# Optimization experiments

Measured on AMD Instinct MI355X. Metric: run time of the kernel, lower is better.

Reference implementation:

```python
import jax, jax.numpy as jnp
import numpy as np

B, IN, H0, H1, OUT = 4096, 1024, 4096, 4096, 1024
QMAX = 127.0


def setup_inputs() -> dict:
    key = jax.random.key(0)
    k0, k1, k2, k3 = jax.random.split(key, 4)
    x = jax.random.normal(k0, (B, IN), dtype=jnp.float32)
    # Linear weights hold already-quantized integer values (module casts .int())
    W0 = jax.random.randint(k1, (H0, IN + 1), -127, 128).astype(jnp.int32)
    W1 = jax.random.randint(k2, (H1, H0 + 1), -127, 128).astype(jnp.int32)
    W2 = jax.random.randint(k3, (OUT, H1 + 1), -127, 128).astype(jnp.int32)
    return {
        "x": x,
        "a_in0": jnp.float32(4.0), "a_w0": jnp.float32(0.05),
        "a_in2": jnp.float32(50.0), "a_w2": jnp.float32(0.05),
        "a_in4": jnp.float32(50.0), "a_w4": jnp.float32(0.05),
        "W0": W0, "W1": W1, "W2": W2,
    }


def _quant(x, amax):
    # clamp(round(x * 127/amax), -127, 127) -> int32
    return jnp.clip(jnp.round(x * (QMAX / amax)), -QMAX, QMAX).astype(jnp.int32)


def _qlinear(x, W, a_in, a_w):
    q = _quant(x, a_in)                                   # [B, K] int32
    ones = jnp.ones((q.shape[0], 1), dtype=jnp.int32)     # folded bias column
    q = jnp.concatenate([q, ones], axis=1)                # [B, K+1]
    acc = q @ W.T                                         # int32 GEMM [B, N]
    return acc.astype(jnp.float32) * (a_w * a_in / (QMAX * QMAX))


def reference(x, a_in0, a_w0, a_in2, a_w2, a_in4, a_w4, W0, W1, W2):
    x = x.reshape(x.shape[0], -1)
    x = _qlinear(x, W0, a_in0, a_w0)
    x = jax.nn.relu(x)
    x = _qlinear(x, W1, a_in2, a_w2)
    x = jax.nn.relu(x)
    x = _qlinear(x, W2, a_in4, a_w4)
    return x
```

## Files before the change

### kernel.cpp

```cpp
#include <hip/hip_runtime.h>

#define QMAX 127.0f

typedef int v4i __attribute__((ext_vector_type(4)));

__device__ __forceinline__ void gload_lds16(const void* g, void* l) {
  __builtin_amdgcn_global_load_lds(
      (const __attribute__((address_space(1))) void*)g,
      (__attribute__((address_space(3))) void*)l, 16, 0, 0);
}

__device__ __forceinline__ void pack_body(const int* __restrict__ W,
                                          signed char* __restrict__ W8,
                                          int* __restrict__ bias,
                                          unsigned lblk, int kshift) {
  unsigned t = lblk * 256u + threadIdx.x;
  unsigned row = t >> kshift;
  unsigned j = t & ((1u << kshift) - 1u);
  unsigned K = 4u << kshift;
  size_t srcBase = (size_t)row * (size_t)(K + 1) + (size_t)j * 4;
  int c0 = W[srcBase + 0], c1 = W[srcBase + 1], c2 = W[srcBase + 2], c3 = W[srcBase + 3];
  unsigned packed = (unsigned)(c0 & 0xff) | ((unsigned)(c1 & 0xff) << 8) |
                    ((unsigned)(c2 & 0xff) << 16) | ((unsigned)(c3 & 0xff) << 24);
  reinterpret_cast<unsigned*>(W8)[t] = packed;
  if (j == 0) bias[row] = W[(size_t)row * (K + 1) + K];
}

__global__ void prep_kernel(const float* __restrict__ x,
                            signed char* __restrict__ qa0,
                            const float* __restrict__ pAin,
                            const int* __restrict__ W0, signed char* __restrict__ W0p, int* __restrict__ b0,
                            const int* __restrict__ W1, signed char* __restrict__ W1p, int* __restrict__ b1,
                            const int* __restrict__ W2, signed char* __restrict__ W2p, int* __restrict__ b2) {
  unsigned blk = blockIdx.x;
  if (blk < 4096u) {
    pack_body(W0, W0p, b0, blk, 8);
  } else if (blk < 20480u) {
    pack_body(W1, W1p, b1, blk - 4096u, 10);
  } else if (blk < 24576u) {
    pack_body(W2, W2p, b2, blk - 20480u, 10);
  } else {
    unsigned t = (blk - 24576u) * 256u + threadIdx.x;
    float s = QMAX / pAin[0];
    float4 v = reinterpret_cast<const float4*>(x)[t];
    int q0 = (int)fminf(fmaxf(rintf(v.x * s), -QMAX), QMAX);
    int q1 = (int)fminf(fmaxf(rintf(v.y * s), -QMAX), QMAX);
    int q2 = (int)fminf(fmaxf(rintf(v.z * s), -QMAX), QMAX);
    int q3 = (int)fminf(fmaxf(rintf(v.w * s), -QMAX), QMAX);
    unsigned packed = (unsigned)(q0 & 0xff) | ((unsigned)(q1 & 0xff) << 8) |
                      ((unsigned)(q2 & 0xff) << 16) | ((unsigned)(q3 & 0xff) << 24);
    reinterpret_cast<unsigned*>(qa0)[t] = packed;
  }
}


#define FENCE() asm volatile("" ::: "memory")
#define BARRIER()                      \
  do {                                 \
    FENCE();                           \
    __builtin_amdgcn_s_barrier();      \
    FENCE();                           \
  } while (0)
#define LGK0() asm volatile("s_waitcnt lgkmcnt(0)" ::: "memory")
#define VMC8() asm volatile("s_waitcnt vmcnt(8)" ::: "memory")
#define VMC0() asm volatile("s_waitcnt vmcnt(0)" ::: "memory")

#define STAGE_A(bf, h, t)                                                     \
  do {                                                                        \
    const signed char* _g = gA + (size_t)((h) * 128) * K + (size_t)(t) * 128; \
    signed char* _l = ldsA + (bf) * 32768 + (h) * 16384 + ldsThr;             \
    gload_lds16(_g, _l);                                                      \
    gload_lds16(_g + (size_t)8 * K, _l + 1024);                               \
  } while (0)

#define STAGE_B(bf, h, t)                                                     \
  do {                                                                        \
    const signed char* _g = gB + (size_t)((h) * 128) * K + (size_t)(t) * 128; \
    signed char* _l = ldsB + (bf) * 32768 + (h) * 16384 + ldsThr;             \
    gload_lds16(_g, _l);                                                      \
    gload_lds16(_g + (size_t)8 * K, _l + 1024);                               \
  } while (0)

#define LDAQ(bf, qm)                                                          \
  do {                                                                        \
    _Pragma("unroll") for (int m = 0; m < 4; ++m) {                           \
      int row = wm * 128 + (qm) * 64 + m * 16 + l15;                          \
      _Pragma("unroll") for (int kk = 0; kk < 2; ++kk) {                      \
        int off = (kk * 64 + hi * 16) ^ ((row & 7) << 4);                     \
        aq[m][kk] = *(const v4i*)(ldsA + (bf) * 32768 + row * 128 + off);     \
      }                                                                       \
    }                                                                         \
  } while (0)

#define LDBF(bf)                                                              \
  do {                                                                        \
    _Pragma("unroll") for (int n = 0; n < 4; ++n) {                           \
      int row = wn * 64 + n * 16 + l15;                                       \
      _Pragma("unroll") for (int kk = 0; kk < 2; ++kk) {                      \
        int off = (kk * 64 + hi * 16) ^ ((row & 7) << 4);                     \
        bR[n][kk] = *(const v4i*)(ldsB + (bf) * 32768 + row * 128 + off);     \
      }                                                                       \
    }                                                                         \
  } while (0)

#define MFMAC(qm)                                                             \
  do {                                                                        \
    __builtin_amdgcn_s_setprio(1);                                            \
    _Pragma("unroll") for (int m = 0; m < 4; ++m)                             \
    _Pragma("unroll") for (int n = 0; n < 4; ++n)                             \
    _Pragma("unroll") for (int kk = 0; kk < 2; ++kk)                          \
      acc[(qm) * 4 + m][n] = __builtin_amdgcn_mfma_i32_16x16x64_i8(           \
          aq[m][kk], bR[n][kk], acc[(qm) * 4 + m][n], 0, 0, 0);               \
    __builtin_amdgcn_s_setprio(0);                                            \
  } while (0)

__global__ __launch_bounds__(512, 2)
void qgemm256_kernel(const signed char* __restrict__ A,
                     const signed char* __restrict__ Bw,
                     const int* __restrict__ bias,
                     signed char* __restrict__ O,
                     int N, int K, int nbn,
                     const float* __restrict__ pAin,
                     const float* __restrict__ pAw,
                     const float* __restrict__ pAnext) {
  extern __shared__ signed char lds[];
  signed char* ldsA = lds;
  signed char* ldsB = lds + 65536;

  const int nwg = gridDim.x, bid = blockIdx.x, per = nwg >> 3;
  const int swz = (bid & 7) * per + (bid >> 3);
  const int brow = swz / nbn, bcol = swz - brow * nbn;
  const int browBase = brow << 8, bcolBase = bcol << 8;

  const int tid = threadIdx.x;
  const int lane = tid & 63, l15 = lane & 15, hi = lane >> 4;
  const int wid = tid >> 6, wm = wid >> 2, wn = wid & 3;

  const int rloc = (wid << 4) + (lane >> 3);
  const int csrc = (lane & 7) ^ ((lane >> 3) & 7);
  const signed char* gA = A + (size_t)(browBase + rloc) * K + csrc * 16;
  const signed char* gB = Bw + (size_t)(bcolBase + rloc) * K + csrc * 16;
  const int ldsThr = (wid << 11) + lane * 16;

  v4i acc[8][4] = {};
  v4i bR[4][2];

  const int nk = K >> 7, niter = nk >> 1, nkm = nk - 1;

  STAGE_B(0, 0, 0); STAGE_B(0, 1, 0); STAGE_A(0, 0, 0); STAGE_A(0, 1, 0);
  STAGE_B(1, 0, 1); STAGE_B(1, 1, 1);

#pragma unroll 1
  for (int i = 0; i < niter; ++i) {
    const int t1 = 2 * i + 1;
    const int tE = (2 * i + 2) & nkm;
    const int tO = (2 * i + 3) & nkm;
    v4i aq[4][2];
    STAGE_A(1, 0, t1); STAGE_A(1, 1, t1);
    VMC8();
    BARRIER();
    LDAQ(0, 0); LDBF(0);
    MFMAC(0);
    LGK0();
    BARRIER();
    STAGE_B(0, 0, tE); STAGE_B(0, 1, tE);
    LDAQ(0, 1);
    MFMAC(1);
    LGK0();
    BARRIER();
    STAGE_A(0, 0, tE); STAGE_A(0, 1, tE);
    VMC8();
    BARRIER();
    LDAQ(1, 0); LDBF(1);
    MFMAC(0);
    LGK0();
    BARRIER();
    STAGE_B(1, 0, tO); STAGE_B(1, 1, tO);
    LDAQ(1, 1);
    MFMAC(1);
    LGK0();
    BARRIER();
  }

  VMC0();

  const float sDeq = (pAw[0] * pAin[0]) / (QMAX * QMAX);
  const float sQ = QMAX / pAnext[0];
#pragma unroll
  for (int nf = 0; nf < 4; ++nf) {
    const int gcol = bcolBase + wn * 64 + nf * 16 + l15;
    const int bv = bias[gcol];
#pragma unroll
    for (int mf = 0; mf < 8; ++mf) {
      const int gr = browBase + wm * 128 + mf * 16 + (hi << 2);
#pragma unroll
      for (int r = 0; r < 4; ++r) {
        float f = (float)(acc[mf][nf][r] + bv) * sDeq;
        f = fmaxf(f, 0.0f);
        float qf = fminf(fmaxf(rintf(f * sQ), -QMAX), QMAX);
        O[(size_t)(gr + r) * N + gcol] = (signed char)(int)qf;
      }
    }
  }
}

__global__ __launch_bounds__(256)
void qgemm_kernel(const signed char* __restrict__ A,
                  const signed char* __restrict__ Bw,
                  const int* __restrict__ bias,
                  float* __restrict__ O,
                  int N, int K, int nbn,
                  const float* __restrict__ pAin,
                  const float* __restrict__ pAw) {
  __shared__ signed char slds[32768];
  signed char* ldsA = slds;
  signed char* ldsB = slds + 16384;

  int nwg = gridDim.x;
  int bid = blockIdx.x;
  int per = nwg >> 3;
  int swz = (bid & 7) * per + (bid >> 3);
  int brow = swz / nbn;
  int bcol = swz - brow * nbn;
  int browBase = brow << 7;
  int bcolBase = bcol << 7;

  int tid = threadIdx.x;
  int lane = tid & 63;
  int l15 = lane & 15;
  int hi = lane >> 4;
  int wid = tid >> 6;
  int wr = (wid >> 1) << 6;
  int wc = (wid & 1) << 6;

  v4i acc[4][4] = {};

  int nk = K >> 7;
  for (int kt = 0; kt < nk; ++kt) {
    int k0 = kt << 7;
#pragma unroll
    for (int i = 0; i < 4; ++i) {
      int c = i * 256 + tid;
      int r = c >> 3;
      int osrc = ((c & 7) << 4) ^ ((r & 7) << 4);
      gload_lds16(A + (size_t)(browBase + r) * K + (k0 + osrc), ldsA + c * 16);
      gload_lds16(Bw + (size_t)(bcolBase + r) * K + (k0 + osrc), ldsB + c * 16);
    }
    __syncthreads();
#pragma unroll
    for (int kk = 0; kk < 2; ++kk) {
      v4i a[4], b[4];
#pragma unroll
      for (int m = 0; m < 4; ++m) {
        int row = wr + m * 16 + l15;
        int off = (kk * 64 + hi * 16) ^ ((row & 7) << 4);
        a[m] = *reinterpret_cast<const v4i*>(ldsA + row * 128 + off);
      }
#pragma unroll
      for (int n = 0; n < 4; ++n) {
        int row = wc + n * 16 + l15;
        int off = (kk * 64 + hi * 16) ^ ((row & 7) << 4);
        b[n] = *reinterpret_cast<const v4i*>(ldsB + row * 128 + off);
      }
#pragma unroll
      for (int m = 0; m < 4; ++m)
#pragma unroll
        for (int n = 0; n < 4; ++n)
          acc[m][n] = __builtin_amdgcn_mfma_i32_16x16x64_i8(a[m], b[n], acc[m][n], 0, 0, 0);
    }
    __syncthreads();
  }

  float sDeq = (pAw[0] * pAin[0]) / (QMAX * QMAX);
#pragma unroll
  for (int n = 0; n < 4; ++n) {
    int gcol = bcolBase + wc + n * 16 + l15;
    int bv = bias[gcol];
#pragma unroll
    for (int m = 0; m < 4; ++m) {
      int growb = browBase + wr + m * 16 + (hi << 2);
#pragma unroll
      for (int r = 0; r < 4; ++r) {
        O[(size_t)(growb + r) * N + gcol] = (float)(acc[m][n][r] + bv) * sDeq;
      }
    }
  }
}

extern "C" void kernel_launch(void* const* d_in, const int* in_sizes, int n_in,
                              void* d_out, int out_size, void* d_ws, size_t ws_size,
                              hipStream_t stream) {
  const float* x     = (const float*)d_in[0];
  const float* a_in0 = (const float*)d_in[1];
  const float* a_w0  = (const float*)d_in[2];
  const float* a_in2 = (const float*)d_in[3];
  const float* a_w2  = (const float*)d_in[4];
  const float* a_in4 = (const float*)d_in[5];
  const float* a_w4  = (const float*)d_in[6];
  const int*   W0    = (const int*)d_in[7];
  const int*   W1    = (const int*)d_in[8];
  const int*   W2    = (const int*)d_in[9];
  float* out = (float*)d_out;

  constexpr int B = 4096, IN = 1024, H0 = 4096, H1 = 4096, OUTN = 1024;

  char* ws = (char*)d_ws;
  size_t off = 0;
  auto alloc = [&](size_t sz) {
    char* p = ws + off;
    off += (sz + 255) & ~(size_t)255;
    return p;
  };
  signed char* qa0 = (signed char*)alloc((size_t)B * IN);
  signed char* qa1 = (signed char*)alloc((size_t)B * H0);
  signed char* qa2 = (signed char*)alloc((size_t)B * H1);
  signed char* W0p = (signed char*)alloc((size_t)H0 * IN);
  signed char* W1p = (signed char*)alloc((size_t)H1 * H0);
  signed char* W2p = (signed char*)alloc((size_t)OUTN * H1);
  int* b0 = (int*)alloc((size_t)H0 * 4);
  int* b1 = (int*)alloc((size_t)H1 * 4);
  int* b2 = (int*)alloc((size_t)OUTN * 4);

  hipFuncSetAttribute((const void*)qgemm256_kernel,
                      hipFuncAttributeMaxDynamicSharedMemorySize, 131072);

  prep_kernel<<<28672, 256, 0, stream>>>(x, qa0, a_in0,
                                         W0, W0p, b0,
                                         W1, W1p, b1,
                                         W2, W2p, b2);

  qgemm256_kernel<<<(B / 256) * (H0 / 256), 512, 131072, stream>>>(
      qa0, W0p, b0, qa1, H0, IN, H0 / 256, a_in0, a_w0, a_in2);

  qgemm256_kernel<<<(B / 256) * (H1 / 256), 512, 131072, stream>>>(
      qa1, W1p, b1, qa2, H1, H0, H1 / 256, a_in2, a_w2, a_in4);

  qgemm_kernel<<<(B / 128) * (OUTN / 128), 256, 0, stream>>>(
      qa2, W2p, b2, out, OUTN, H1, OUTN / 128, a_in4, a_w4);
}
```

Baseline: 142.9 us.

## Restructure GEMM pipelines with register double-buffered A fragments and LDS ping-pong

Rewrites the main loop of the 256-tile kernel to stage whole K-tiles (A and B together) into alternating LDS buffers. A fragments are double-buffered in registers (aK0/aK1) so LDS reads for the next half-K slice overlap the current MFMA block. The 128-tile output kernel gets the same treatment: double-buffered LDS (64KB) and register-prefetched fragments replace the previous single-buffer loop with __syncthreads around each tile. This is meant to hide global and LDS latency behind MFMA work, at the cost of more registers and LDS. The tight lgkmcnt/vmcnt waits also risk subtle race bugs.

```diff
diff --git a/kernel.cpp b/kernel.cpp
--- a/kernel.cpp
+++ b/kernel.cpp
@@ -61,8 +61,7 @@
     __builtin_amdgcn_s_barrier();      \
     FENCE();                           \
   } while (0)
-#define LGK0() asm volatile("s_waitcnt lgkmcnt(0)" ::: "memory")
-#define VMC8() asm volatile("s_waitcnt vmcnt(8)" ::: "memory")
+#define LGK(n) asm volatile("s_waitcnt lgkmcnt(" #n ")" ::: "memory")
 #define VMC0() asm volatile("s_waitcnt vmcnt(0)" ::: "memory")
 
 #define STAGE_A(bf, h, t)                                                     \
@@ -81,36 +80,37 @@
     gload_lds16(_g + (size_t)8 * K, _l + 1024);                               \
   } while (0)
 
-#define LDAQ(bf, qm)                                                          \
-  do {                                                                        \
-    _Pragma("unroll") for (int m = 0; m < 4; ++m) {                           \
-      int row = wm * 128 + (qm) * 64 + m * 16 + l15;                          \
-      _Pragma("unroll") for (int kk = 0; kk < 2; ++kk) {                      \
-        int off = (kk * 64 + hi * 16) ^ ((row & 7) << 4);                     \
-        aq[m][kk] = *(const v4i*)(ldsA + (bf) * 32768 + row * 128 + off);     \
-      }                                                                       \
-    }                                                                         \
-  } while (0)
-
-#define LDBF(bf)                                                              \
+#define STAGE_T(bf, t)                                                        \
+  do {                                                                        \
+    STAGE_A(bf, 0, t); STAGE_A(bf, 1, t);                                     \
+    STAGE_B(bf, 0, t); STAGE_B(bf, 1, t);                                     \
+  } while (0)
+
+#define LDA8(bf, kk, dst)                                                     \
+  do {                                                                        \
+    _Pragma("unroll") for (int m = 0; m < 8; ++m) {                           \
+      int row = wm * 128 + m * 16 + l15;                                      \
+      int off = ((kk) * 64 + hi * 16) ^ ((l15 & 7) << 4);                     \
+      dst[m] = *(const v4i*)(ldsA + (bf) * 32768 + row * 128 + off);          \
+    }                                                                         \
+  } while (0)
+
+#define LDB4(bf, kk)                                                          \
   do {                                                                        \
     _Pragma("unroll") for (int n = 0; n < 4; ++n) {                           \
       int row = wn * 64 + n * 16 + l15;                                       \
-      _Pragma("unroll") for (int kk = 0; kk < 2; ++kk) {                      \
-        int off = (kk * 64 + hi * 16) ^ ((row & 7) << 4);                     \
-        bR[n][kk] = *(const v4i*)(ldsB + (bf) * 32768 + row * 128 + off);     \
-      }                                                                       \
-    }                                                                         \
-  } while (0)
-
-#define MFMAC(qm)                                                             \
+      int off = ((kk) * 64 + hi * 16) ^ ((l15 & 7) << 4);                     \
+      bK[n] = *(const v4i*)(ldsB + (bf) * 32768 + row * 128 + off);           \
+    }                                                                         \
+  } while (0)
+
+#define MFMA32(aset)                                                          \
   do {                                                                        \
     __builtin_amdgcn_s_setprio(1);                                            \
-    _Pragma("unroll") for (int m = 0; m < 4; ++m)                             \
+    _Pragma("unroll") for (int m = 0; m < 8; ++m)                             \
     _Pragma("unroll") for (int n = 0; n < 4; ++n)                             \
-    _Pragma("unroll") for (int kk = 0; kk < 2; ++kk)                          \
-      acc[(qm) * 4 + m][n] = __builtin_amdgcn_mfma_i32_16x16x64_i8(           \
-          aq[m][kk], bR[n][kk], acc[(qm) * 4 + m][n], 0, 0, 0);               \
+      acc[m][n] = __builtin_amdgcn_mfma_i32_16x16x64_i8(                      \
+          aset[m], bK[n], acc[m][n], 0, 0, 0);                                \
     __builtin_amdgcn_s_setprio(0);                                            \
   } while (0)
 
@@ -143,43 +143,41 @@
   const int ldsThr = (wid << 11) + lane * 16;
 
   v4i acc[8][4] = {};
-  v4i bR[4][2];
+  v4i aK0[8], aK1[8], bK[4];
 
   const int nk = K >> 7, niter = nk >> 1, nkm = nk - 1;
 
-  STAGE_B(0, 0, 0); STAGE_B(0, 1, 0); STAGE_A(0, 0, 0); STAGE_A(0, 1, 0);
-  STAGE_B(1, 0, 1); STAGE_B(1, 1, 1);
+  STAGE_T(0, 0);
+  VMC0();
+  BARRIER();
+  LDA8(0, 0, aK0);
 
 #pragma unroll 1
   for (int i = 0; i < niter; ++i) {
-    const int t1 = 2 * i + 1;
+    const int tO = 2 * i + 1;
     const int tE = (2 * i + 2) & nkm;
-    const int tO = (2 * i + 3) & nkm;
-    v4i aq[4][2];
-    STAGE_A(1, 0, t1); STAGE_A(1, 1, t1);
-    VMC8();
-    BARRIER();
-    LDAQ(0, 0); LDBF(0);
-    MFMAC(0);
-    LGK0();
-    BARRIER();
-    STAGE_B(0, 0, tE); STAGE_B(0, 1, tE);
-    LDAQ(0, 1);
-    MFMAC(1);
-    LGK0();
-    BARRIER();
-    STAGE_A(0, 0, tE); STAGE_A(0, 1, tE);
-    VMC8();
-    BARRIER();
-    LDAQ(1, 0); LDBF(1);
-    MFMAC(0);
-    LGK0();
-    BARRIER();
-    STAGE_B(1, 0, tO); STAGE_B(1, 1, tO);
-    LDAQ(1, 1);
-    MFMAC(1);
-    LGK0();
-    BARRIER();
+    LGK(8);
+    BARRIER();
+    STAGE_T(1, tO);
+    LDB4(0, 0); FENCE(); LDA8(0, 1, aK1);
+    LGK(8);
+    MFMA32(aK0);
+    VMC0();
+    BARRIER();
+    LDB4(0, 1); FENCE(); LDA8(1, 0, aK0);
+    LGK(8);
+    MFMA32(aK1);
+    LGK(8);
+    BARRIER();
+    STAGE_T(0, tE);
+    LDB4(1, 0); FENCE(); LDA8(1, 1, aK1);
+    LGK(8);
+    MFMA32(aK0);
+    VMC0();
+    BARRIER();
+    LDB4(1, 1); FENCE(); LDA8(0, 0, aK0);
+    LGK(8);
+    MFMA32(aK1);
   }
 
   VMC0();
@@ -203,6 +201,47 @@
     }
   }
 }
+
+#define STG128(bf, t)                                                         \
+  do {                                                                        \
+    _Pragma("unroll") for (int ii = 0; ii < 4; ++ii) {                        \
+      int c = ii * 256 + tid;                                                 \
+      int r = c >> 3;                                                         \
+      int osrc = ((c & 7) << 4) ^ ((r & 7) << 4);                             \
+      gload_lds16(A + (size_t)(browBase + r) * K + ((t) * 128 + osrc),        \
+                  ldsA + (bf) * 16384 + c * 16);                              \
+      gload_lds16(Bw + (size_t)(bcolBase + r) * K + ((t) * 128 + osrc),       \
+                  ldsB + (bf) * 16384 + c * 16);                              \
+    }                                                                         \
+  } while (0)
+
+#define LDA4_128(bf, kk, dst)                                                 \
+  do {                                                                        \
+    _Pragma("unroll") for (int m = 0; m < 4; ++m) {                           \
+      int row = wr + m * 16 + l15;                                            \
+      int off = ((kk) * 64 + hi * 16) ^ ((l15 & 7) << 4);                     \
+      dst[m] = *(const v4i*)(ldsA + (bf) * 16384 + row * 128 + off);          \
+    }                                                                         \
+  } while (0)
+
+#define LDB4_128(bf, kk)                                                      \
+  do {                                                                        \
+    _Pragma("unroll") for (int n = 0; n < 4; ++n) {                           \
+      int row = wc + n * 16 + l15;                                            \
+      int off = ((kk) * 64 + hi * 16) ^ ((l15 & 7) << 4);                     \
+      bK[n] = *(const v4i*)(ldsB + (bf) * 16384 + row * 128 + off);           \
+    }                                                                         \
+  } while (0)
+
+#define MFMA16(aset)                                                          \
+  do {                                                                        \
+    __builtin_amdgcn_s_setprio(1);                                            \
+    _Pragma("unroll") for (int m = 0; m < 4; ++m)                             \
+    _Pragma("unroll") for (int n = 0; n < 4; ++n)                             \
+      acc[m][n] = __builtin_amdgcn_mfma_i32_16x16x64_i8(                      \
+          aset[m], bK[n], acc[m][n], 0, 0, 0);                                \
+    __builtin_amdgcn_s_setprio(0);                                            \
+  } while (0)
 
 __global__ __launch_bounds__(256)
 void qgemm_kernel(const signed char* __restrict__ A,
@@ -212,66 +251,61 @@
                   int N, int K, int nbn,
                   const float* __restrict__ pAin,
                   const float* __restrict__ pAw) {
-  __shared__ signed char slds[32768];
+  __shared__ signed char slds[65536];
   signed char* ldsA = slds;
-  signed char* ldsB = slds + 16384;
-
-  int nwg = gridDim.x;
-  int bid = blockIdx.x;
-  int per = nwg >> 3;
-  int swz = (bid & 7) * per + (bid >> 3);
-  int brow = swz / nbn;
-  int bcol = swz - brow * nbn;
-  int browBase = brow << 7;
-  int bcolBase = bcol << 7;
-
-  int tid = threadIdx.x;
-  int lane = tid & 63;
-  int l15 = lane & 15;
-  int hi = lane >> 4;
-  int wid = tid >> 6;
-  int wr = (wid >> 1) << 6;
-  int wc = (wid & 1) << 6;
+  signed char* ldsB = slds + 32768;
+
+  const int nwg = gridDim.x, bid = blockIdx.x, per = nwg >> 3;
+  const int swz = (bid & 7) * per + (bid >> 3);
+  const int brow = swz / nbn, bcol = swz - brow * nbn;
+  const int browBase = brow << 7, bcolBase = bcol << 7;
+
+  const int tid = threadIdx.x;
+  const int lane = tid & 63, l15 = lane & 15, hi = lane >> 4;
+  const int wid = tid >> 6;
+  const int wr = (wid >> 1) << 6, wc = (wid & 1) << 6;
 
   v4i acc[4][4] = {};
-
-  int nk = K >> 7;
-  for (int kt = 0; kt < nk; ++kt) {
-    int k0 = kt << 7;
-#pragma unroll
-    for (int i = 0; i < 4; ++i) {
-      int c = i * 256 + tid;
-      int r = c >> 3;
-      int osrc = ((c & 7) << 4) ^ ((r & 7) << 4);
-      gload_lds16(A + (size_t)(browBase + r) * K + (k0 + osrc), ldsA + c * 16);
-      gload_lds16(Bw + (size_t)(bcolBase + r) * K + (k0 + osrc), ldsB + c * 16);
-    }
-    __syncthreads();
-#pragma unroll
-    for (int kk = 0; kk < 2; ++kk) {
-      v4i a[4], b[4];
-#pragma unroll
-      for (int m = 0; m < 4; ++m) {
-        int row = wr + m * 16 + l15;
-        int off = (kk * 64 + hi * 16) ^ ((row & 7) << 4);
-        a[m] = *reinterpret_cast<const v4i*>(ldsA + row * 128 + off);
-      }
-#pragma unroll
-      for (int n = 0; n < 4; ++n) {
-        int row = wc + n * 16 + l15;
-        int off = (kk * 64 + hi * 16) ^ ((row & 7) << 4);
-        b[n] = *reinterpret_cast<const v4i*>(ldsB + row * 128 + off);
-      }
-#pragma unroll
-      for (int m = 0; m < 4; ++m)
-#pragma unroll
-        for (int n = 0; n < 4; ++n)
-          acc[m][n] = __builtin_amdgcn_mfma_i32_16x16x64_i8(a[m], b[n], acc[m][n], 0, 0, 0);
-    }
-    __syncthreads();
-  }
-
-  float sDeq = (pAw[0] * pAin[0]) / (QMAX * QMAX);
+  v4i aK0[4], aK1[4], bK[4];
+
+  const int nk = K >> 7, niter = nk >> 1, nkm = nk - 1;
+
+  STG128(0, 0);
+  VMC0();
+  BARRIER();
+  LDA4_128(0, 0, aK0);
+
+#pragma unroll 1
+  for (int i = 0; i < niter; ++i) {
+    const int tO = 2 * i + 1;
+    const int tE = (2 * i + 2) & nkm;
+    LGK(4);
+    BARRIER();
+    STG128(1, tO);
+    LDB4_128(0, 0); FENCE(); LDA4_128(0, 1, aK1);
+    LGK(4);
+    MFMA16(aK0);
+    VMC0();
+    BARRIER();
+    LDB4_128(0, 1); FENCE(); LDA4_128(1, 0, aK0);
+    LGK(4);
+    MFMA16(aK1);
+    LGK(4);
+    BARRIER();
+    STG128(0, tE);
+    LDB4_128(1, 0); FENCE(); LDA4_128(1, 1, aK1);
+    LGK(4);
+    MFMA16(aK0);
+    VMC0();
+    BARRIER();
+    LDB4_128(1, 1); FENCE(); LDA4_128(0, 0, aK0);
+    LGK(4);
+    MFMA16(aK1);
+  }
+
+  VMC0();
+
+  const float sDeq = (pAw[0] * pAin[0]) / (QMAX * QMAX);
 #pragma unroll
   for (int n = 0; n < 4; ++n) {
     int gcol = bcolBase + wc + n * 16 + l15;
```

After: 139.9 us. 2.1% less time.
